# Performance work log

Measured on AMD Instinct MI355X. Metric: run time of the kernel, lower is better.

The kernel has to match this reference:

```python
import jax, jax.numpy as jnp
import numpy as np

B, S, E, D, L, H = 8, 1024, 512, 1024, 8, 16
HD = D // H                 # 64
ROT = max(HD // 2, 32)      # 32
FF = 4 * D
FUSED = 3 * D + 2 * FF      # q,k,v,ff,ff_gate
EPS = 1e-5


def layer_norm(x, w, b):
    mu = jnp.mean(x, axis=-1, keepdims=True)
    var = jnp.mean(jnp.square(x - mu), axis=-1, keepdims=True)
    return (x - mu) * jax.lax.rsqrt(var + EPS) * w + b


def gelu(x):  # fused_gelu from source (erf form, constant 1.41421)
    return x * 0.5 * (1.0 + jax.scipy.special.erf(x / 1.41421))


def silu(x):
    return x * jax.nn.sigmoid(x)


def rotate_half(x):
    x1, x2 = jnp.split(x, 2, axis=-1)
    return jnp.concatenate([-x2, x1], axis=-1)


def rope_tables(seq_len):
    inv = 1.0 / (10000.0 ** (jnp.arange(0, ROT, 2, dtype=jnp.float32) / ROT))
    freqs = jnp.arange(seq_len, dtype=jnp.float32)[:, None] * inv[None, :]
    emb = jnp.concatenate([freqs, freqs], axis=-1)  # [S, ROT]
    # source caches sin/cos in bfloat16 (precision=torch.bfloat16)
    sin = jnp.sin(emb).astype(jnp.bfloat16).astype(jnp.float32)[None, None]
    cos = jnp.cos(emb).astype(jnp.bfloat16).astype(jnp.float32)[None, None]
    return sin, cos  # [1,1,S,ROT]


def setup_inputs() -> dict:
    key = jax.random.key(0)
    ks = jax.random.split(key, 24)
    std = 0.02
    inp = {
        "noisy_embeds": jax.random.normal(ks[0], (B, S, E), jnp.float32),
        "cond_embeds": jax.random.normal(ks[1], (B, S, E), jnp.float32),
        "prev_embeds": jax.random.normal(ks[2], (B, S, E), jnp.float32),
        "infill_mask": jax.random.uniform(ks[3], (B, S, 1), jnp.float32),
        "attention_mask": jnp.zeros((B, 1, 1, S), jnp.float32),
        "times": jax.random.uniform(ks[4], (B,), jnp.float32),
        # time embedding params
        "fourier_w": jax.random.normal(ks[5], (D // 2, 1), jnp.float32),
        "t1_w": jax.random.normal(ks[6], (D, D), jnp.float32) * std,
        "t1_b": jnp.zeros((D,), jnp.float32),
        "t2_w": jax.random.normal(ks[7], (D, D), jnp.float32) * std,
        "t2_b": jnp.zeros((D,), jnp.float32),
        # input projection
        "in_w": jax.random.normal(ks[8], (D, 4 * E), jnp.float32) * std,
        "in_b": jnp.zeros((D,), jnp.float32),
        # per-layer (stacked) block params
        "ln_w": jnp.ones((L, D), jnp.float32),
        "ln_b": jnp.zeros((L, D), jnp.float32),
        "cond_w": jax.random.normal(ks[9], (L, 2 * D, D), jnp.float32) * std,
        "cond_b": jnp.zeros((L, 2 * D), jnp.float32),
        "proj_w": jax.random.normal(ks[10], (L, FUSED, D), jnp.float32) * std,
        "attn_w": jax.random.normal(ks[11], (L, D, D), jnp.float32) * std,
        "attn_b": jnp.zeros((L, D), jnp.float32),
        "ff_w": jax.random.normal(ks[12], (L, D, FF), jnp.float32) * std,
        "ff_b": jnp.zeros((L, D), jnp.float32),
        # output head
        "outln_w": jnp.ones((D,), jnp.float32),
        "outln_b": jnp.zeros((D,), jnp.float32),
        "out_w": jax.random.normal(ks[13], (E, D), jnp.float32) * std,
        "out_b": jnp.zeros((E,), jnp.float32),
        "fin_w": jnp.ones((E,), jnp.float32),
        "fin_b": jnp.zeros((E,), jnp.float32),
    }
    return inp


def _split_heads(x):  # [B,S,H*hd] -> [B,H,S,hd]
    return x.reshape(B, S, H, HD).transpose(0, 2, 1, 3)


def _forward(noisy_embeds, cond_embeds, prev_embeds, infill_mask, attention_mask,
             times, fourier_w, t1_w, t1_b, t2_w, t2_b, in_w, in_b,
             ln_w, ln_b, cond_w, cond_b, proj_w, attn_w, attn_b, ff_w, ff_b,
             outln_w, outln_b, out_w, out_b, fin_w, fin_b):
    # -- time embedding (Random Fourier + MLP) --
    f = 2.0 * np.pi * (times[:, None] @ fourier_w.T)          # [B, D/2]
    te = jnp.concatenate([jnp.cos(f), jnp.sin(f)], axis=-1)   # [B, D]
    te = gelu(te @ t1_w.T + t1_b) @ t2_w.T + t2_b             # [B, D]
    time_embeds = te[:, None, :]                              # [B, 1, D]

    # -- input projection: cat(noisy, cond, prev, mask broadcast) --
    mask_feat = infill_mask * jnp.ones_like(noisy_embeds)     # [B,S,E]
    x = jnp.concatenate([noisy_embeds, cond_embeds, prev_embeds, mask_feat], axis=-1)
    h = x @ in_w.T + in_b                                     # [B,S,D]

    sin, cos = rope_tables(S)
    sm_scale = HD ** (-0.5)

    for i in range(L):
        units = layer_norm(h, ln_w[i], ln_b[i])
        # FiLM conditioning
        sb = silu(time_embeds) @ cond_w[i].T + cond_b[i]      # [B,1,2D]
        scale, bias = jnp.split(sb, 2, axis=-1)
        units = (1.0 + scale) * units + bias
        # fused projection and split
        proj = units @ proj_w[i].T                            # [B,S,11D]
        q, k, v, ff, ff_gate = jnp.split(
            proj, np.cumsum([D, D, D, FF])[:4].tolist(), axis=-1)
        q, k, v = _split_heads(q), _split_heads(k), _split_heads(v)  # [B,H,S,hd]
        # rotary on first ROT dims
        q = jnp.concatenate(
            [q[..., :ROT] * cos + rotate_half(q[..., :ROT]) * sin, q[..., ROT:]], axis=-1)
        k = jnp.concatenate(
            [k[..., :ROT] * cos + rotate_half(k[..., :ROT]) * sin, k[..., ROT:]], axis=-1)
        # NOTE: source scales BOTH q and k by hd^-0.5 (effective hd^-1)
        score = jnp.einsum('bhsd,bhSd->bhsS', q * sm_scale, k * sm_scale)
        score = score + attention_mask
        w = jax.nn.softmax(score, axis=-1)
        attn = jnp.einsum('bhsS,bhSd->bhsd', w, v)
        merged = attn.transpose(0, 2, 1, 3).reshape(B, S, D)
        attn_out = merged @ attn_w[i].T + attn_b[i]
        ff_out = (ff * gelu(ff_gate)) @ ff_w[i].T + ff_b[i]
        h = h + attn_out + ff_out

    out = layer_norm(h, outln_w, outln_b) @ out_w.T + out_b   # [B,S,E]
    return layer_norm(out, fin_w, fin_b)


def reference(noisy_embeds, cond_embeds, prev_embeds, infill_mask, attention_mask,
              times, fourier_w, t1_w, t1_b, t2_w, t2_b, in_w, in_b,
              ln_w, ln_b, cond_w, cond_b, proj_w, attn_w, attn_b, ff_w, ff_b,
              outln_w, outln_b, out_w, out_b, fin_w, fin_b):
    return _forward(noisy_embeds, cond_embeds, prev_embeds, infill_mask, attention_mask,
                    times, fourier_w, t1_w, t1_b, t2_w, t2_b, in_w, in_b,
                    ln_w, ln_b, cond_w, cond_b, proj_w, attn_w, attn_b, ff_w, ff_b,
                    outln_w, outln_b, out_w, out_b, fin_w, fin_b)
```

## Files before the change

### kernel.cpp

```cpp
#include <hip/hip_runtime.h>
#include <hip/hip_bf16.h>
#include <cstddef>
#include <cstdint>

#define BB 8
#define SS 1024
#define EE 512
#define DD 1024
#define LL 8
#define HH 16
#define HD 64
#define ROT 32
#define FF 4096
#define FUSED 11264
#define NTOK 8192
#define QKVW 3072
#define CATW 5120

using u16 = unsigned short;
typedef __attribute__((ext_vector_type(8))) __bf16 bf16x8;
typedef __attribute__((ext_vector_type(4))) float f32x4;
typedef __attribute__((ext_vector_type(4))) unsigned short u16x4;
typedef __attribute__((ext_vector_type(8))) unsigned short u16x8;

typedef const __attribute__((address_space(1))) void gas_t;
typedef __attribute__((address_space(3))) void las_t;

#define VMCNT8 asm volatile("s_waitcnt vmcnt(8)" ::: "memory")
#define VMCNT0 asm volatile("s_waitcnt vmcnt(0)" ::: "memory")

__device__ __forceinline__ void gld16(const void* g, void* l) {
  __builtin_amdgcn_global_load_lds((gas_t*)g, (las_t*)l, 16, 0, 0);
}

__device__ __forceinline__ float bf2f(u16 u) {
  union { unsigned int i; float f; } v; v.i = ((unsigned int)u) << 16; return v.f;
}
__device__ __forceinline__ u16 f2bf(float f) {
  union { float f; unsigned int i; } v; v.f = f;
  unsigned int u = v.i;
  unsigned int r = u + 0x7FFFu + ((u >> 16) & 1u);
  return (u16)(r >> 16);
}
__device__ __forceinline__ float gelu_f(float x) {
  return x * 0.5f * (1.0f + erff(x / 1.41421f));
}
__device__ __forceinline__ float silu_f(float x) {
  return x / (1.0f + __expf(-x));
}

template <int ACCUM, int OUTBF16>
__global__ __launch_bounds__(256, 2) void gemm_bt(
    const u16* __restrict__ A, const u16* __restrict__ W,
    const float* __restrict__ bias, void* __restrict__ Cp,
    int M, int N, int K) {
  __shared__ __align__(16) u16 As[2][128 * 64];
  __shared__ __align__(16) u16 Bs[2][128 * 64];
  const int tid = threadIdx.x;
  const int w = tid >> 6, lane = tid & 63;
  const int m0 = blockIdx.y * 128, n0 = blockIdx.x * 128;
  const int wm = w >> 1, wn = w & 1;

  f32x4 acc[4][4] = {};

  auto stage = [&](int buf, int k0) {
#pragma unroll
    for (int i = 0; i < 4; i++) {
      const int c = w + i * 4;
      const int r = c * 8 + (lane >> 3);
      const int colb = ((lane & 7) << 4) ^ ((r & 7) << 4);
      gld16(A + (size_t)(m0 + r) * K + k0 + (colb >> 1), &As[buf][c * 512]);
      gld16(W + (size_t)(n0 + r) * K + k0 + (colb >> 1), &Bs[buf][c * 512]);
    }
  };

  const int nt = K >> 6;
  stage(0, 0);

  for (int t = 0; t < nt; t++) {
    const int cur = t & 1;
    if (t + 1 < nt) {
      stage(cur ^ 1, (t + 1) << 6);
      VMCNT8;
    } else {
      VMCNT0;
    }
    __builtin_amdgcn_s_barrier();

    bf16x8 av0[4], bv0[4], av1[4], bv1[4];
#pragma unroll
    for (int m = 0; m < 4; m++) {
      const int row = wm * 64 + m * 16 + (lane & 15);
      const int sw = (row & 7) << 4;
      av0[m] = *(const bf16x8*)((const char*)As[cur] + row * 128 + ((((lane >> 4) << 4)) ^ sw));
      av1[m] = *(const bf16x8*)((const char*)As[cur] + row * 128 + ((64 + ((lane >> 4) << 4)) ^ sw));
    }
#pragma unroll
    for (int n = 0; n < 4; n++) {
      const int row = wn * 64 + n * 16 + (lane & 15);
      const int sw = (row & 7) << 4;
      bv0[n] = *(const bf16x8*)((const char*)Bs[cur] + row * 128 + ((((lane >> 4) << 4)) ^ sw));
      bv1[n] = *(const bf16x8*)((const char*)Bs[cur] + row * 128 + ((64 + ((lane >> 4) << 4)) ^ sw));
    }
    __builtin_amdgcn_s_setprio(1);
#pragma unroll
    for (int m = 0; m < 4; m++)
#pragma unroll
      for (int n = 0; n < 4; n++)
        acc[m][n] = __builtin_amdgcn_mfma_f32_16x16x32_bf16(av0[m], bv0[n], acc[m][n], 0, 0, 0);
#pragma unroll
    for (int m = 0; m < 4; m++)
#pragma unroll
      for (int n = 0; n < 4; n++)
        acc[m][n] = __builtin_amdgcn_mfma_f32_16x16x32_bf16(av1[m], bv1[n], acc[m][n], 0, 0, 0);
    __builtin_amdgcn_s_setprio(0);
    __builtin_amdgcn_s_barrier();
  }

  const int rowb0 = m0 + wm * 64 + ((lane >> 4) << 2);
  const int colb0 = n0 + wn * 64 + (lane & 15);
#pragma unroll
  for (int n = 0; n < 4; n++) {
    const int col = colb0 + n * 16;
    const float bn = bias ? bias[col] : 0.0f;
#pragma unroll
    for (int m = 0; m < 4; m++) {
#pragma unroll
      for (int r = 0; r < 4; r++) {
        const size_t idx = (size_t)(rowb0 + m * 16 + r) * N + col;
        const float v = acc[m][n][r] + bn;
        if (ACCUM) {
          ((float*)Cp)[idx] += v;
        } else if (OUTBF16) {
          ((u16*)Cp)[idx] = f2bf(v);
        } else {
          ((float*)Cp)[idx] = v;
        }
      }
    }
  }
}

template <int GATED>
__global__ __launch_bounds__(512, 2) void gemm_bt256(
    const u16* __restrict__ A, const u16* __restrict__ W,
    void* __restrict__ Cp, int M, int N, int K, int ostride, int ocol0) {
  __shared__ __align__(16) u16 As[2][256 * 64];
  __shared__ __align__(16) u16 Bs[2][256 * 64];
  const int tid = threadIdx.x;
  const int w = tid >> 6, lane = tid & 63;
  const int m0 = blockIdx.y * 256, n0 = blockIdx.x * 256;
  const int wm = w >> 2, wn = w & 3;

  f32x4 acc[8][4] = {};

  auto stage = [&](int buf, int k0) {
#pragma unroll
    for (int i = 0; i < 4; i++) {
      const int c = w + i * 8;
      const int r = c * 8 + (lane >> 3);
      const int colb = ((lane & 7) << 4) ^ ((r & 7) << 4);
      gld16(A + (size_t)(m0 + r) * K + k0 + (colb >> 1), &As[buf][c * 512]);
      gld16(W + (size_t)(n0 + r) * K + k0 + (colb >> 1), &Bs[buf][c * 512]);
    }
  };

  const int nt = K >> 6;
  stage(0, 0);

  for (int t = 0; t < nt; t++) {
    const int cur = t & 1;
    if (t + 1 < nt) {
      stage(cur ^ 1, (t + 1) << 6);
      VMCNT8;
    } else {
      VMCNT0;
    }
    __builtin_amdgcn_s_barrier();

    {
      bf16x8 av0[8], bv0[4];
#pragma unroll
      for (int m = 0; m < 8; m++) {
        const int row = wm * 128 + m * 16 + (lane & 15);
        const int cb = (((lane >> 4) << 4)) ^ ((row & 7) << 4);
        av0[m] = *(const bf16x8*)((const char*)As[cur] + row * 128 + cb);
      }
#pragma unroll
      for (int n = 0; n < 4; n++) {
        const int row = wn * 64 + n * 16 + (lane & 15);
        const int cb = (((lane >> 4) << 4)) ^ ((row & 7) << 4);
        bv0[n] = *(const bf16x8*)((const char*)Bs[cur] + row * 128 + cb);
      }
      __builtin_amdgcn_s_setprio(1);
#pragma unroll
      for (int m = 0; m < 8; m++)
#pragma unroll
        for (int n = 0; n < 4; n++)
          acc[m][n] = __builtin_amdgcn_mfma_f32_16x16x32_bf16(av0[m], bv0[n], acc[m][n], 0, 0, 0);
      __builtin_amdgcn_s_setprio(0);
    }
    {
      bf16x8 av1[8], bv1[4];
#pragma unroll
      for (int m = 0; m < 8; m++) {
        const int row = wm * 128 + m * 16 + (lane & 15);
        const int cb = (64 + ((lane >> 4) << 4)) ^ ((row & 7) << 4);
        av1[m] = *(const bf16x8*)((const char*)As[cur] + row * 128 + cb);
      }
#pragma unroll
      for (int n = 0; n < 4; n++) {
        const int row = wn * 64 + n * 16 + (lane & 15);
        const int cb = (64 + ((lane >> 4) << 4)) ^ ((row & 7) << 4);
        bv1[n] = *(const bf16x8*)((const char*)Bs[cur] + row * 128 + cb);
      }
      __builtin_amdgcn_s_setprio(1);
#pragma unroll
      for (int m = 0; m < 8; m++)
#pragma unroll
        for (int n = 0; n < 4; n++)
          acc[m][n] = __builtin_amdgcn_mfma_f32_16x16x32_bf16(av1[m], bv1[n], acc[m][n], 0, 0, 0);
      __builtin_amdgcn_s_setprio(0);
    }
    __builtin_amdgcn_s_barrier();
  }

  const int rowb0 = m0 + wm * 128 + ((lane >> 4) << 2);
  if (GATED) {
#pragma unroll
    for (int n = 0; n < 4; n += 2) {
      const int outcol = (n0 >> 1) + wn * 32 + ((n >> 1) << 4) + (lane & 15);
#pragma unroll
      for (int m = 0; m < 8; m++)
#pragma unroll
        for (int r = 0; r < 4; r++) {
          const float fv = acc[m][n][r];
          const float gv = acc[m][n + 1][r];
          ((u16*)Cp)[(size_t)(rowb0 + m * 16 + r) * ostride + ocol0 + outcol] =
              f2bf(fv * gelu_f(gv));
        }
    }
  } else {
    const int colb0 = n0 + wn * 64 + (lane & 15);
#pragma unroll
    for (int n = 0; n < 4; n++) {
      const int col = colb0 + n * 16;
#pragma unroll
      for (int m = 0; m < 8; m++)
#pragma unroll
        for (int r = 0; r < 4; r++)
          ((u16*)Cp)[(size_t)(rowb0 + m * 16 + r) * ostride + ocol0 + col] = f2bf(acc[m][n][r]);
    }
  }
}

__global__ __launch_bounds__(256, 2) void attn_fwd(
    const u16* __restrict__ qr, const u16* __restrict__ kr,
    const u16* __restrict__ vt, const float* __restrict__ mask,
    u16* __restrict__ acat) {
  __shared__ __align__(16) u16 Ks[2][128 * 64];
  __shared__ __align__(16) u16 Vs[2][64 * 128];
  __shared__ __align__(16) u16 Ps[4][16 * 128];
  const int tid = threadIdx.x, w = tid >> 6, lane = tid & 63;
  const int g = blockIdx.x;
  const int j = g >> 3;
  const int bh = (g & 7) + ((j >> 4) << 3);
  const int qx = j & 15;
  const int b = bh >> 4;
  const int q0 = qx * 64 + w * 16;
  const u16* Qb = qr + (size_t)bh * SS * HD;
  const u16* Kb = kr + (size_t)bh * SS * HD;
  const u16* Vb = vt + (size_t)bh * HD * SS;
  const float* mb = mask + (size_t)b * SS;
  const int lq = lane & 15, lg = lane >> 4;

  bf16x8 qf0, qf1;
  {
    const int qrow = q0 + lq;
    const u16* qp = Qb + (size_t)qrow * HD + (lg << 3);
    qf0 = *(const bf16x8*)qp;
    qf1 = *(const bf16x8*)(qp + 32);
  }

  float mrun = -1e30f, srun = 0.0f;
  f32x4 acc[4] = {};

  u16* pw = &Ps[w][0];

  auto stage = [&](int buf, int kv0) {
#pragma unroll
    for (int i = 0; i < 4; i++) {
      const int c = w + i * 4;
      {
        const int r = c * 8 + (lane >> 3);
        const int colb = ((lane & 7) << 4) ^ ((r & 7) << 4);
        gld16(Kb + (size_t)(kv0 + r) * HD + (colb >> 1), &Ks[buf][c * 512]);
      }
      {
        const int d = c * 4 + lg;
        const int colb = (lq << 4) ^ ((d & 7) << 4);
        gld16(Vb + (size_t)d * SS + kv0 + (colb >> 1), &Vs[buf][c * 512]);
      }
    }
  };

  stage(0, 0);
  __syncthreads();

  for (int t = 0; t < 8; t++) {
    const int cur = t & 1;
    const int kv0 = t * 128;
    if (t < 7) stage(cur ^ 1, kv0 + 128);

    f32x4 p[8];
    __builtin_amdgcn_s_setprio(1);
#pragma unroll
    for (int blk = 0; blk < 8; blk++) {
      const int row = blk * 16 + lq;
      const int swz = (row & 7) << 4;
      const bf16x8 k0v = *(const bf16x8*)((const char*)Ks[cur] + row * 128 + (((lg << 4)) ^ swz));
      const bf16x8 k1v = *(const bf16x8*)((const char*)Ks[cur] + row * 128 + ((64 + (lg << 4)) ^ swz));
      f32x4 z = {};
      p[blk] = __builtin_amdgcn_mfma_f32_16x16x32_bf16(k0v, qf0, z, 0, 0, 0);
      p[blk] = __builtin_amdgcn_mfma_f32_16x16x32_bf16(k1v, qf1, p[blk], 0, 0, 0);
    }
    __builtin_amdgcn_s_setprio(0);

#pragma unroll
    for (int blk = 0; blk < 8; blk++) {
      const float4 m4 = *(const float4*)(mb + kv0 + blk * 16 + (lg << 2));
      p[blk][0] = p[blk][0] * (1.0f / 64.0f) + m4.x;
      p[blk][1] = p[blk][1] * (1.0f / 64.0f) + m4.y;
      p[blk][2] = p[blk][2] * (1.0f / 64.0f) + m4.z;
      p[blk][3] = p[blk][3] * (1.0f / 64.0f) + m4.w;
    }

    float mr[8];
#pragma unroll
    for (int blk = 0; blk < 8; blk++)
      mr[blk] = fmaxf(fmaxf(p[blk][0], p[blk][1]), fmaxf(p[blk][2], p[blk][3]));
    float mrow = fmaxf(fmaxf(fmaxf(mr[0], mr[1]), fmaxf(mr[2], mr[3])),
                       fmaxf(fmaxf(mr[4], mr[5]), fmaxf(mr[6], mr[7])));
    mrow = fmaxf(mrow, __shfl_xor(mrow, 16));
    mrow = fmaxf(mrow, __shfl_xor(mrow, 32));

    if (__any(mrow > mrun)) {
      const float mn = fmaxf(mrun, mrow);
      const float facq = __expf(mrun - mn);
      mrun = mn;
      srun *= facq;
      float fac[4];
#pragma unroll
      for (int r = 0; r < 4; r++)
        fac[r] = __shfl(facq, (lane & 48) | ((lg << 2) + r));
#pragma unroll
      for (int dblk = 0; dblk < 4; dblk++)
#pragma unroll
        for (int r = 0; r < 4; r++) acc[dblk][r] *= fac[r];
    }

    float rs0 = 0.0f, rs1 = 0.0f, rs2 = 0.0f, rs3 = 0.0f;
#pragma unroll
    for (int blk = 0; blk < 8; blk++) {
      const float e0 = __expf(p[blk][0] - mrun);
      const float e1 = __expf(p[blk][1] - mrun);
      const float e2 = __expf(p[blk][2] - mrun);
      const float e3 = __expf(p[blk][3] - mrun);
      rs0 += e0; rs1 += e1; rs2 += e2; rs3 += e3;
      unsigned int r01, r23;
      asm("v_cvt_pk_bf16_f32 %0, %1, %2" : "=v"(r01) : "v"(e0), "v"(e1));
      asm("v_cvt_pk_bf16_f32 %0, %1, %2" : "=v"(r23) : "v"(e2), "v"(e3));
      uint2 pk; pk.x = r01; pk.y = r23;
      *(uint2*)(pw + ((lq * 128 + blk * 16 + (lg << 2)) ^ ((lq & 7) << 3))) = pk;
    }
    float rs = (rs0 + rs1) + (rs2 + rs3);
    rs += __shfl_xor(rs, 16);
    rs += __shfl_xor(rs, 32);
    srun += rs;

    bf16x8 pa[4];
#pragma unroll
    for (int ks = 0; ks < 4; ks++)
      pa[ks] = *(const bf16x8*)(pw + ((lq * 128 + ks * 32 + (lg << 3)) ^ ((lq & 7) << 3)));

    __builtin_amdgcn_s_setprio(1);
#pragma unroll
    for (int dblk = 0; dblk < 4; dblk++) {
      const int drow = dblk * 16 + lq;
      const int swz = (drow & 7) << 4;
#pragma unroll
      for (int ks = 0; ks < 4; ks++) {
        const bf16x8 vv = *(const bf16x8*)((const char*)Vs[cur] + drow * 256 + ((ks * 64 + (lg << 4)) ^ swz));
        acc[dblk] = __builtin_amdgcn_mfma_f32_16x16x32_bf16(pa[ks], vv, acc[dblk], 0, 0, 0);
      }
    }
    __builtin_amdgcn_s_setprio(0);

    __syncthreads();
  }

  float sden[4];
#pragma unroll
  for (int r = 0; r < 4; r++)
    sden[r] = __shfl(srun, (lane & 48) | ((lg << 2) + r));
#pragma unroll
  for (int dblk = 0; dblk < 4; dblk++)
#pragma unroll
    for (int r = 0; r < 4; r++) {
      const int sq = q0 + (lg << 2) + r;
      const int d = dblk * 16 + lq;
      acat[((size_t)b * SS + sq) * CATW + (bh & 15) * HD + d] = f2bf(acc[dblk][r] / sden[r]);
    }
}

__global__ __launch_bounds__(256) void ln_mod(
    const float* __restrict__ x, const float* __restrict__ lw,
    const float* __restrict__ lb, const float* __restrict__ sb,
    u16* __restrict__ out) {
  const int row = blockIdx.x, tid = threadIdx.x;
  const float4 v = ((const float4*)(x + (size_t)row * DD))[tid];
  float vv[4] = {v.x, v.y, v.z, v.w};
  float s = vv[0] + vv[1] + vv[2] + vv[3];
  float q = vv[0] * vv[0] + vv[1] * vv[1] + vv[2] * vv[2] + vv[3] * vv[3];
  for (int off = 1; off < 64; off <<= 1) {
    s += __shfl_xor(s, off);
    q += __shfl_xor(q, off);
  }
  __shared__ float red[8];
  const int w = tid >> 6, lane = tid & 63;
  if (lane == 0) { red[w] = s; red[4 + w] = q; }
  __syncthreads();
  s = red[0] + red[1] + red[2] + red[3];
  q = red[4] + red[5] + red[6] + red[7];
  const float mu = s * (1.0f / DD);
  const float inv = rsqrtf(q * (1.0f / DD) - mu * mu + 1e-5f);
  const int b = row >> 10;
  u16x4 o;
#pragma unroll
  for (int j = 0; j < 4; j++) {
    const int d = tid * 4 + j;
    float g = (vv[j] - mu) * inv * lw[d] + lb[d];
    if (sb) g = (1.0f + sb[(size_t)b * 2048 + d]) * g + sb[(size_t)b * 2048 + DD + d];
    o[j] = f2bf(g);
  }
  *(u16x4*)(out + (size_t)row * DD + tid * 4) = o;
}

__global__ __launch_bounds__(128) void ln_fin(
    const float* __restrict__ x, const float* __restrict__ w_,
    const float* __restrict__ b_, float* __restrict__ out) {
  const int row = blockIdx.x, tid = threadIdx.x;
  const float4 v = ((const float4*)(x + (size_t)row * EE))[tid];
  float vv[4] = {v.x, v.y, v.z, v.w};
  float s = vv[0] + vv[1] + vv[2] + vv[3];
  float q = vv[0] * vv[0] + vv[1] * vv[1] + vv[2] * vv[2] + vv[3] * vv[3];
  for (int off = 1; off < 64; off <<= 1) {
    s += __shfl_xor(s, off);
    q += __shfl_xor(q, off);
  }
  __shared__ float red[4];
  const int w = tid >> 6, lane = tid & 63;
  if (lane == 0) { red[w] = s; red[2 + w] = q; }
  __syncthreads();
  s = red[0] + red[1];
  q = red[2] + red[3];
  const float mu = s * (1.0f / EE);
  const float inv = rsqrtf(q * (1.0f / EE) - mu * mu + 1e-5f);
  float4 o;
  o.x = (vv[0] - mu) * inv * w_[tid * 4 + 0] + b_[tid * 4 + 0];
  o.y = (vv[1] - mu) * inv * w_[tid * 4 + 1] + b_[tid * 4 + 1];
  o.z = (vv[2] - mu) * inv * w_[tid * 4 + 2] + b_[tid * 4 + 2];
  o.w = (vv[3] - mu) * inv * w_[tid * 4 + 3] + b_[tid * 4 + 3];
  ((float4*)(out + (size_t)row * EE))[tid] = o;
}

template <int IA, int OA>
__global__ __launch_bounds__(256) void vec_gemm(
    const float* __restrict__ in, const float* __restrict__ W,
    const float* __restrict__ bias, float* __restrict__ out, int N, int K) {
  const int n = blockIdx.x * 256 + threadIdx.x;
  const int b = blockIdx.y, l = blockIdx.z;
  const float* ir = in + (size_t)b * K;
  const float* wr = W + ((size_t)l * N + n) * K;
  float s = bias[(size_t)l * N + n];
  for (int k = 0; k < K; k += 4) {
    float4 a = *(const float4*)(ir + k);
    const float4 ww = *(const float4*)(wr + k);
    if (IA) { a.x = silu_f(a.x); a.y = silu_f(a.y); a.z = silu_f(a.z); a.w = silu_f(a.w); }
    s += a.x * ww.x + a.y * ww.y + a.z * ww.z + a.w * ww.w;
  }
  if (OA) s = gelu_f(s);
  out[((size_t)l * gridDim.y + b) * N + n] = s;
}

__global__ void time_fourier(const float* __restrict__ times,
                             const float* __restrict__ fw, float* __restrict__ te0) {
  const int j = blockIdx.x * 256 + threadIdx.x;
  const int b = blockIdx.y;
  const float f = 6.28318530717958647692f * times[b] * fw[j];
  te0[(size_t)b * DD + j] = cosf(f);
  te0[(size_t)b * DD + 512 + j] = sinf(f);
}

__global__ void rope_tab(float* __restrict__ st, float* __restrict__ ct) {
  const int s = blockIdx.x;
  const int j = threadIdx.x;
  const int i = j & 15;
  const float inv = powf(10000.0f, -(float)i * (1.0f / 16.0f));
  const float f = (float)s * inv;
  st[s * 32 + j] = bf2f(f2bf(sinf(f)));
  ct[s * 32 + j] = bf2f(f2bf(cosf(f)));
}

__global__ void build_x(const float* __restrict__ a, const float* __restrict__ b,
                        const float* __restrict__ c, const float* __restrict__ m,
                        u16* __restrict__ x) {
  const size_t i4 = ((size_t)blockIdx.x * 256 + threadIdx.x) * 4;
  if (i4 >= (size_t)NTOK * 2048) return;
  const size_t tok = i4 >> 11;
  const int e = (int)(i4 & 2047);
  float4 v;
  if (e < 512)       v = *(const float4*)(a + tok * 512 + e);
  else if (e < 1024) v = *(const float4*)(b + tok * 512 + (e - 512));
  else if (e < 1536) v = *(const float4*)(c + tok * 512 + (e - 1024));
  else { const float mm = m[tok]; v = make_float4(mm, mm, mm, mm); }
  u16x4 o;
  o[0] = f2bf(v.x); o[1] = f2bf(v.y); o[2] = f2bf(v.z); o[3] = f2bf(v.w);
  *(u16x4*)(x + i4) = o;
}

__global__ __launch_bounds__(256) void rope_all(
    const u16* __restrict__ proj, const float* __restrict__ st,
    const float* __restrict__ ct, u16* __restrict__ q, u16* __restrict__ k,
    u16* __restrict__ v) {
  __shared__ u16 tile[4 * 1160];
  const int tid = threadIdx.x;
  const int s0 = blockIdx.x * 64, h = blockIdx.y, b = blockIdx.z;
  const int sl = tid >> 2, c = tid & 3;
  const int s = s0 + sl;
  const u16* pr = proj + (size_t)(b * SS + s) * QKVW + h * 64;

  {
    const u16x8 a0 = *(const u16x8*)(pr + 2 * DD + c * 16);
    const u16x8 a1 = *(const u16x8*)(pr + 2 * DD + c * 16 + 8);
    u16* trow = &tile[(sl >> 4) * 1160 + (sl & 15) * 72];
    *(u16x8*)&trow[c * 16] = a0;
    *(u16x8*)&trow[c * 16 + 8] = a1;
  }

  {
    const int d0 = c * 16;
    u16 qv[16], kv[16], qo[16], ko[16];
    *(u16x8*)&qv[0] = *(const u16x8*)(pr + d0);
    *(u16x8*)&qv[8] = *(const u16x8*)(pr + d0 + 8);
    *(u16x8*)&kv[0] = *(const u16x8*)(pr + DD + d0);
    *(u16x8*)&kv[8] = *(const u16x8*)(pr + DD + d0 + 8);
    if (c < 2) {
      const int dp = (c ^ 1) * 16;
      u16 qp[16], kp[16];
      *(u16x8*)&qp[0] = *(const u16x8*)(pr + dp);
      *(u16x8*)&qp[8] = *(const u16x8*)(pr + dp + 8);
      *(u16x8*)&kp[0] = *(const u16x8*)(pr + DD + dp);
      *(u16x8*)&kp[8] = *(const u16x8*)(pr + DD + dp + 8);
      const float sg = (c == 0) ? -1.0f : 1.0f;
#pragma unroll
      for (int j = 0; j < 16; j++) {
        const int d = d0 + j;
        const float cs = ct[s * 32 + d], sn = st[s * 32 + d];
        qo[j] = f2bf(bf2f(qv[j]) * cs + sg * bf2f(qp[j]) * sn);
        ko[j] = f2bf(bf2f(kv[j]) * cs + sg * bf2f(kp[j]) * sn);
      }
    } else {
#pragma unroll
      for (int j = 0; j < 16; j++) { qo[j] = qv[j]; ko[j] = kv[j]; }
    }
    u16* qd = q + ((size_t)(b * HH + h) * SS + s) * HD + d0;
    u16* kd = k + ((size_t)(b * HH + h) * SS + s) * HD + d0;
    *(u16x8*)qd = *(u16x8*)&qo[0];
    *(u16x8*)(qd + 8) = *(u16x8*)&qo[8];
    *(u16x8*)kd = *(u16x8*)&ko[0];
    *(u16x8*)(kd + 8) = *(u16x8*)&ko[8];
  }

  __syncthreads();

  {
    const int dl = tid >> 2, gq = tid & 3;
    const u16* tg = &tile[gq * 1160];
    u16x8 o0, o1;
#pragma unroll
    for (int j = 0; j < 8; j++) o0[j] = tg[j * 72 + dl];
#pragma unroll
    for (int j = 0; j < 8; j++) o1[j] = tg[(8 + j) * 72 + dl];
    u16* dst = v + ((size_t)(b * HH + h) * HD + dl) * SS + s0 + gq * 16;
    *(u16x8*)dst = o0;
    *(u16x8*)(dst + 8) = o1;
  }
}

__global__ void cast_bf16(const float* __restrict__ in, u16* __restrict__ out, size_t n4) {
  const size_t i = (size_t)blockIdx.x * 256 + threadIdx.x;
  if (i >= n4) return;
  const float4 v = ((const float4*)in)[i];
  u16x4 o;
  o[0] = f2bf(v.x); o[1] = f2bf(v.y); o[2] = f2bf(v.z); o[3] = f2bf(v.w);
  ((u16x4*)out)[i] = o;
}

__global__ void cast_q(const float* __restrict__ src, u16* __restrict__ dst) {
  const int i = blockIdx.x * 256 + threadIdx.x;
  const int l = blockIdx.y;
  const int r = i >> 7, cb = (i & 127) * 8;
  const float* s = src + ((size_t)l * FUSED + r) * DD + cb;
  const float4 a = *(const float4*)s;
  const float4 b = *(const float4*)(s + 4);
  u16x8 o;
  o[0] = f2bf(a.x); o[1] = f2bf(a.y); o[2] = f2bf(a.z); o[3] = f2bf(a.w);
  o[4] = f2bf(b.x); o[5] = f2bf(b.y); o[6] = f2bf(b.z); o[7] = f2bf(b.w);
  *(u16x8*)(dst + ((size_t)l * QKVW + r) * DD + cb) = o;
}

__global__ void cast_ffg(const float* __restrict__ src, u16* __restrict__ dst) {
  const int i = blockIdx.x * 256 + threadIdx.x;
  const int l = blockIdx.y;
  const int r = i >> 7, cb = (i & 127) * 8;
  const int t16 = r >> 4, pos = r & 15;
  const int j = (t16 >> 1) * 16 + pos;
  const int srow = (t16 & 1) ? (3 * DD + FF + j) : (3 * DD + j);
  const float* s = src + ((size_t)l * FUSED + srow) * DD + cb;
  const float4 a = *(const float4*)s;
  const float4 b = *(const float4*)(s + 4);
  u16x8 o;
  o[0] = f2bf(a.x); o[1] = f2bf(a.y); o[2] = f2bf(a.z); o[3] = f2bf(a.w);
  o[4] = f2bf(b.x); o[5] = f2bf(b.y); o[6] = f2bf(b.z); o[7] = f2bf(b.w);
  *(u16x8*)(dst + ((size_t)l * 8192 + r) * DD + cb) = o;
}

__global__ void cast_catw(const float* __restrict__ aw, const float* __restrict__ fw,
                          u16* __restrict__ dst) {
  const int i = blockIdx.x * 256 + threadIdx.x;
  const int l = blockIdx.y;
  const int n = i / 640, cb = (i % 640) * 8;
  const float* s = (cb < DD) ? (aw + ((size_t)l * DD + n) * DD + cb)
                             : (fw + ((size_t)l * DD + n) * FF + (cb - DD));
  const float4 a = *(const float4*)s;
  const float4 b = *(const float4*)(s + 4);
  u16x8 o;
  o[0] = f2bf(a.x); o[1] = f2bf(a.y); o[2] = f2bf(a.z); o[3] = f2bf(a.w);
  o[4] = f2bf(b.x); o[5] = f2bf(b.y); o[6] = f2bf(b.z); o[7] = f2bf(b.w);
  *(u16x8*)(dst + ((size_t)l * DD + n) * CATW + cb) = o;
}

__global__ void add_bias(const float* __restrict__ a, const float* __restrict__ b,
                         float* __restrict__ o, int n) {
  const int i = blockIdx.x * 256 + threadIdx.x;
  if (i < n) o[i] = a[i] + b[i];
}

extern "C" void kernel_launch(void* const* d_in, const int* in_sizes, int n_in,
                              void* d_out, int out_size, void* d_ws, size_t ws_size,
                              hipStream_t stream) {
  const float* noisy   = (const float*)d_in[0];
  const float* condi   = (const float*)d_in[1];
  const float* prev    = (const float*)d_in[2];
  const float* infill  = (const float*)d_in[3];
  const float* amask   = (const float*)d_in[4];
  const float* times   = (const float*)d_in[5];
  const float* fourier = (const float*)d_in[6];
  const float* t1_w    = (const float*)d_in[7];
  const float* t1_b    = (const float*)d_in[8];
  const float* t2_w    = (const float*)d_in[9];
  const float* t2_b    = (const float*)d_in[10];
  const float* in_w    = (const float*)d_in[11];
  const float* in_b    = (const float*)d_in[12];
  const float* ln_w    = (const float*)d_in[13];
  const float* ln_b    = (const float*)d_in[14];
  const float* cond_w  = (const float*)d_in[15];
  const float* cond_b  = (const float*)d_in[16];
  const float* proj_w  = (const float*)d_in[17];
  const float* attn_w  = (const float*)d_in[18];
  const float* attn_b  = (const float*)d_in[19];
  const float* ff_w    = (const float*)d_in[20];
  const float* ff_b    = (const float*)d_in[21];
  const float* outln_w = (const float*)d_in[22];
  const float* outln_b = (const float*)d_in[23];
  const float* out_w   = (const float*)d_in[24];
  const float* out_b   = (const float*)d_in[25];
  const float* fin_w   = (const float*)d_in[26];
  const float* fin_b   = (const float*)d_in[27];
  float* outp = (float*)d_out;

  char* p = (char*)d_ws;
  auto alloc = [&](size_t bytes) -> char* {
    char* r = p;
    p += (bytes + 255) & ~(size_t)255;
    return r;
  };
  u16* in_w_h    = (u16*)alloc((size_t)DD * 2048 * 2);
  u16* projq_w_h = (u16*)alloc((size_t)LL * QKVW * DD * 2);
  u16* ffg_w_h   = (u16*)alloc((size_t)LL * 8192 * DD * 2);
  u16* cat_w_h   = (u16*)alloc((size_t)LL * DD * CATW * 2);
  float* cat_b   = (float*)alloc((size_t)LL * DD * 4);
  u16* out_w_h   = (u16*)alloc((size_t)EE * DD * 2);
  float* te0 = (float*)alloc((size_t)BB * DD * 4);
  float* te1 = (float*)alloc((size_t)BB * DD * 4);
  float* te2 = (float*)alloc((size_t)BB * DD * 4);
  float* sb  = (float*)alloc((size_t)LL * BB * 2048 * 4);
  float* stab = (float*)alloc((size_t)SS * 32 * 4);
  float* ctab = (float*)alloc((size_t)SS * 32 * 4);
  u16* xb    = (u16*)alloc((size_t)NTOK * 2048 * 2);
  float* h   = (float*)alloc((size_t)NTOK * DD * 4);
  u16* units = (u16*)alloc((size_t)NTOK * DD * 2);
  u16* projq = (u16*)alloc((size_t)NTOK * QKVW * 2);
  u16* qrb   = (u16*)alloc((size_t)NTOK * DD * 2);
  u16* krb   = (u16*)alloc((size_t)NTOK * DD * 2);
  u16* vtb   = (u16*)alloc((size_t)NTOK * DD * 2);
  u16* acat  = (u16*)alloc((size_t)NTOK * CATW * 2);
  u16* hn    = (u16*)alloc((size_t)NTOK * DD * 2);
  float* ob  = (float*)alloc((size_t)NTOK * EE * 4);

  auto castN = [&](const float* src, u16* dst, size_t n) {
    const size_t n4 = n / 4;
    cast_bf16<<<dim3((unsigned)((n4 + 255) / 256)), dim3(256), 0, stream>>>(src, dst, n4);
  };
  castN(in_w, in_w_h, (size_t)DD * 2048);
  cast_q<<<dim3(QKVW * 128 / 256, LL), 256, 0, stream>>>(proj_w, projq_w_h);
  cast_ffg<<<dim3(8192 * 128 / 256, LL), 256, 0, stream>>>(proj_w, ffg_w_h);
  cast_catw<<<dim3(DD * 640 / 256, LL), 256, 0, stream>>>(attn_w, ff_w, cat_w_h);
  add_bias<<<dim3(LL * DD / 256), 256, 0, stream>>>(attn_b, ff_b, cat_b, LL * DD);
  castN(out_w, out_w_h, (size_t)EE * DD);

  time_fourier<<<dim3(2, BB), 256, 0, stream>>>(times, fourier, te0);
  vec_gemm<0, 1><<<dim3(4, BB, 1), 256, 0, stream>>>(te0, t1_w, t1_b, te1, 1024, 1024);
  vec_gemm<0, 0><<<dim3(4, BB, 1), 256, 0, stream>>>(te1, t2_w, t2_b, te2, 1024, 1024);
  vec_gemm<1, 0><<<dim3(8, BB, LL), 256, 0, stream>>>(te2, cond_w, cond_b, sb, 2048, 1024);
  rope_tab<<<SS, 32, 0, stream>>>(stab, ctab);
  build_x<<<16384, 256, 0, stream>>>(noisy, condi, prev, infill, xb);
  gemm_bt<0, 0><<<dim3(DD / 128, NTOK / 128), 256, 0, stream>>>(xb, in_w_h, in_b, h, NTOK, DD, 2048);

  for (int l = 0; l < LL; l++) {
    ln_mod<<<NTOK, 256, 0, stream>>>(h, ln_w + (size_t)l * DD, ln_b + (size_t)l * DD,
                                     sb + (size_t)l * BB * 2048, units);
    gemm_bt<0, 1><<<dim3(QKVW / 128, NTOK / 128), 256, 0, stream>>>(
        units, projq_w_h + (size_t)l * QKVW * DD, nullptr, projq, NTOK, QKVW, DD);
    gemm_bt256<1><<<dim3(8192 / 256, NTOK / 256), 512, 0, stream>>>(
        units, ffg_w_h + (size_t)l * 8192 * DD, acat, NTOK, 8192, DD, CATW, DD);
    rope_all<<<dim3(SS / 64, HH, BB), 256, 0, stream>>>(projq, stab, ctab, qrb, krb, vtb);
    attn_fwd<<<dim3(2048), 256, 0, stream>>>(qrb, krb, vtb, amask, acat);
    gemm_bt<1, 0><<<dim3(DD / 128, NTOK / 128), 256, 0, stream>>>(
        acat, cat_w_h + (size_t)l * DD * CATW, cat_b + (size_t)l * DD, h, NTOK, DD, CATW);
  }

  ln_mod<<<NTOK, 256, 0, stream>>>(h, outln_w, outln_b, nullptr, hn);
  gemm_bt<0, 0><<<dim3(EE / 128, NTOK / 128), 256, 0, stream>>>(hn, out_w_h, out_b, ob, NTOK, EE, DD);
  ln_fin<<<NTOK, 128, 0, stream>>>(ob, fin_w, fin_b, outp);
}
```

Measured before the change: 4.634 ms.

## Fuse QKV projection and gated FF GEMMs into one 256-tile launch

Merges the QKV projection GEMM (previously run with the 128-tile kernel) and the gated feed-forward GEMM into a single 256x256-tile kernel over a concatenated bf16 weight matrix of width FUSED. Blocks whose column tile lies past the QKV width write the gelu-gated output into the concat buffer, and the rest write plain QKV. This removes one launch per layer, moves the QKV part onto the larger, more efficient tile, and improves tail utilisation by giving the grid more blocks. The weight cast kernels now write into one combined layout. The trade-off is a branch in the epilogue.

```diff
diff --git a/kernel.cpp b/kernel.cpp
--- a/kernel.cpp
+++ b/kernel.cpp
@@ -141,10 +141,9 @@
   }
 }
 
-template <int GATED>
-__global__ __launch_bounds__(512, 2) void gemm_bt256(
+__global__ __launch_bounds__(512, 2) void gemm_qf256(
     const u16* __restrict__ A, const u16* __restrict__ W,
-    void* __restrict__ Cp, int M, int N, int K, int ostride, int ocol0) {
+    u16* __restrict__ projq, u16* __restrict__ acat, int M, int K) {
   __shared__ __align__(16) u16 As[2][256 * 64];
   __shared__ __align__(16) u16 Bs[2][256 * 64];
   const int tid = threadIdx.x;
@@ -226,18 +225,18 @@
   }
 
   const int rowb0 = m0 + wm * 128 + ((lane >> 4) << 2);
-  if (GATED) {
+  if (n0 >= QKVW) {
+    const int ocol0 = DD + ((n0 - QKVW) >> 1);
 #pragma unroll
     for (int n = 0; n < 4; n += 2) {
-      const int outcol = (n0 >> 1) + wn * 32 + ((n >> 1) << 4) + (lane & 15);
+      const int outcol = ocol0 + wn * 32 + ((n >> 1) << 4) + (lane & 15);
 #pragma unroll
       for (int m = 0; m < 8; m++)
 #pragma unroll
         for (int r = 0; r < 4; r++) {
           const float fv = acc[m][n][r];
           const float gv = acc[m][n + 1][r];
-          ((u16*)Cp)[(size_t)(rowb0 + m * 16 + r) * ostride + ocol0 + outcol] =
-              f2bf(fv * gelu_f(gv));
+          acat[(size_t)(rowb0 + m * 16 + r) * CATW + outcol] = f2bf(fv * gelu_f(gv));
         }
     }
   } else {
@@ -249,7 +248,7 @@
       for (int m = 0; m < 8; m++)
 #pragma unroll
         for (int r = 0; r < 4; r++)
-          ((u16*)Cp)[(size_t)(rowb0 + m * 16 + r) * ostride + ocol0 + col] = f2bf(acc[m][n][r]);
+          projq[(size_t)(rowb0 + m * 16 + r) * QKVW + col] = f2bf(acc[m][n][r]);
     }
   }
 }
@@ -617,7 +616,7 @@
   u16x8 o;
   o[0] = f2bf(a.x); o[1] = f2bf(a.y); o[2] = f2bf(a.z); o[3] = f2bf(a.w);
   o[4] = f2bf(b.x); o[5] = f2bf(b.y); o[6] = f2bf(b.z); o[7] = f2bf(b.w);
-  *(u16x8*)(dst + ((size_t)l * QKVW + r) * DD + cb) = o;
+  *(u16x8*)(dst + ((size_t)l * FUSED + r) * DD + cb) = o;
 }
 
 __global__ void cast_ffg(const float* __restrict__ src, u16* __restrict__ dst) {
@@ -633,7 +632,7 @@
   u16x8 o;
   o[0] = f2bf(a.x); o[1] = f2bf(a.y); o[2] = f2bf(a.z); o[3] = f2bf(a.w);
   o[4] = f2bf(b.x); o[5] = f2bf(b.y); o[6] = f2bf(b.z); o[7] = f2bf(b.w);
-  *(u16x8*)(dst + ((size_t)l * 8192 + r) * DD + cb) = o;
+  *(u16x8*)(dst + ((size_t)l * FUSED + QKVW + r) * DD + cb) = o;
 }
 
 __global__ void cast_catw(const float* __restrict__ aw, const float* __restrict__ fw,
@@ -697,8 +696,7 @@
     return r;
   };
   u16* in_w_h    = (u16*)alloc((size_t)DD * 2048 * 2);
-  u16* projq_w_h = (u16*)alloc((size_t)LL * QKVW * DD * 2);
-  u16* ffg_w_h   = (u16*)alloc((size_t)LL * 8192 * DD * 2);
+  u16* qf_w_h    = (u16*)alloc((size_t)LL * FUSED * DD * 2);
   u16* cat_w_h   = (u16*)alloc((size_t)LL * DD * CATW * 2);
   float* cat_b   = (float*)alloc((size_t)LL * DD * 4);
   u16* out_w_h   = (u16*)alloc((size_t)EE * DD * 2);
@@ -724,8 +722,8 @@
     cast_bf16<<<dim3((unsigned)((n4 + 255) / 256)), dim3(256), 0, stream>>>(src, dst, n4);
   };
   castN(in_w, in_w_h, (size_t)DD * 2048);
-  cast_q<<<dim3(QKVW * 128 / 256, LL), 256, 0, stream>>>(proj_w, projq_w_h);
-  cast_ffg<<<dim3(8192 * 128 / 256, LL), 256, 0, stream>>>(proj_w, ffg_w_h);
+  cast_q<<<dim3(QKVW * 128 / 256, LL), 256, 0, stream>>>(proj_w, qf_w_h);
+  cast_ffg<<<dim3(8192 * 128 / 256, LL), 256, 0, stream>>>(proj_w, qf_w_h);
   cast_catw<<<dim3(DD * 640 / 256, LL), 256, 0, stream>>>(attn_w, ff_w, cat_w_h);
   add_bias<<<dim3(LL * DD / 256), 256, 0, stream>>>(attn_b, ff_b, cat_b, LL * DD);
   castN(out_w, out_w_h, (size_t)EE * DD);
@@ -741,10 +739,8 @@
   for (int l = 0; l < LL; l++) {
     ln_mod<<<NTOK, 256, 0, stream>>>(h, ln_w + (size_t)l * DD, ln_b + (size_t)l * DD,
                                      sb + (size_t)l * BB * 2048, units);
-    gemm_bt<0, 1><<<dim3(QKVW / 128, NTOK / 128), 256, 0, stream>>>(
-        units, projq_w_h + (size_t)l * QKVW * DD, nullptr, projq, NTOK, QKVW, DD);
-    gemm_bt256<1><<<dim3(8192 / 256, NTOK / 256), 512, 0, stream>>>(
-        units, ffg_w_h + (size_t)l * 8192 * DD, acat, NTOK, 8192, DD, CATW, DD);
+    gemm_qf256<<<dim3(FUSED / 256, NTOK / 256), 512, 0, stream>>>(
+        units, qf_w_h + (size_t)l * FUSED * DD, projq, acat, NTOK, DD);
     rope_all<<<dim3(SS / 64, HH, BB), 256, 0, stream>>>(projq, stab, ctab, qrb, krb, vtb);
     attn_fwd<<<dim3(2048), 256, 0, stream>>>(qrb, krb, vtb, amask, acat);
     gemm_bt<1, 0><<<dim3(DD / 128, NTOK / 128), 256, 0, stream>>>(
```

New measurement: 4.651 ms. About the same (+0.4%).
